# Optimization experiments

Hardware: AMD Instinct MI355X
Metric: run time of the kernel (lower is better)

## Reference

```python
import jax, jax.numpy as jnp
import numpy as np

N = 50000      # n_nodes
E = 600000     # n_edges (avg degree 12)
IN_DIM = 128
HID = 256
OUT = 2


def _glorot(k, fan_in, fan_out):
    s = jnp.sqrt(6.0 / (fan_in + fan_out))
    return jax.random.uniform(k, (fan_in, fan_out), jnp.float32, -s, s)


def setup_inputs() -> dict:
    key = jax.random.key(0)
    ks = jax.random.split(key, 6)
    x = jax.random.normal(ks[0], (N, IN_DIM), jnp.float32)
    edge_index = jax.random.randint(ks[1], (2, E), 0, N, jnp.int32)
    W1 = _glorot(ks[2], IN_DIM, HID)
    b1 = jnp.zeros((HID,), jnp.float32)
    W2 = _glorot(ks[3], HID, HID)
    b2 = jnp.zeros((HID,), jnp.float32)
    Wl = _glorot(ks[4], HID, OUT)
    bl = jnp.zeros((OUT,), jnp.float32)
    return {"x": x, "edge_index": edge_index, "W1": W1, "b1": b1,
            "W2": W2, "b2": b2, "Wl": Wl, "bl": bl}


def _gcn_conv(x, W, b, src, dst, dinv, n):
    # PyG GCNConv: transform, then propagate with symmetric norm + self-loops.
    h = x @ W                                   # [N, F_out]
    norm = (dinv[src] * dinv[dst])[:, None]     # [E, 1]
    agg = jax.ops.segment_sum(h[src] * norm, dst, num_segments=n)
    agg = agg + h * (dinv * dinv)[:, None]      # self-loop term: deg^-1 * h
    return agg + b


def reference(x, edge_index, W1, b1, W2, b2, Wl, bl):
    n = x.shape[0]
    src, dst = edge_index[0], edge_index[1]
    # degree (with self-loop) computed on destination nodes, as in PyG gcn_norm
    deg = jax.ops.segment_sum(jnp.ones((src.shape[0],), jnp.float32), dst,
                              num_segments=n) + 1.0
    dinv = jax.lax.rsqrt(deg)
    h = jax.nn.relu(_gcn_conv(x, W1, b1, src, dst, dinv, n))
    # dropout is identity in eval mode
    h = jax.nn.relu(_gcn_conv(h, W2, b2, src, dst, dinv, n))
    return h @ Wl + bl
```

## Files before the change

### kernel.cpp

```cpp
#include <hip/hip_runtime.h>
#include <hip/hip_bf16.h>
#include <hip/hip_fp16.h>

constexpr int IN_DIM = 128;
constexpr int HID    = 256;

typedef _Float16 f16x8 __attribute__((ext_vector_type(8)));
typedef float    f32x4 __attribute__((ext_vector_type(4)));


__global__ void zero_deg(int* __restrict__ deg, int n) {
    int i = blockIdx.x * blockDim.x + threadIdx.x;
    if (i < n) deg[i] = 0;
}

__device__ inline void conv_B_elem(const float* B, ushort* Bp, int id) {
    int k  = id >> 6;
    int n4 = (id & 63) * 4;
    float4 v = *(const float4*)(B + (size_t)k * 256 + n4);
    size_t base = (size_t)(k >> 5) * (256 * 32) + (k & 31);
    Bp[base + (size_t)(n4 + 0) * 32] = __half_as_ushort(__float2half(v.x));
    Bp[base + (size_t)(n4 + 1) * 32] = __half_as_ushort(__float2half(v.y));
    Bp[base + (size_t)(n4 + 2) * 32] = __half_as_ushort(__float2half(v.z));
    Bp[base + (size_t)(n4 + 3) * 32] = __half_as_ushort(__float2half(v.w));
}

__global__ void convert_count(const float* __restrict__ W1, ushort* __restrict__ B1p,
                              const float* __restrict__ W2, ushort* __restrict__ B2p,
                              const float* __restrict__ x, ushort* __restrict__ xh,
                              int total4, const int* __restrict__ dst,
                              int* __restrict__ rank, int* __restrict__ deg, int e) {
    int id = blockIdx.x * 256 + threadIdx.x;
    constexpr int C1 = IN_DIM * 64;
    constexpr int C2 = C1 + HID * 64;
    if (id < C1) {
        conv_B_elem(W1, B1p, id);
    } else if (id < C2) {
        conv_B_elem(W2, B2p, id - C1);
    } else if (id < C2 + total4) {
        int i = id - C2;
        float4 v = *(const float4*)(x + (size_t)i * 4);
        ushort4 o;
        o.x = __half_as_ushort(__float2half(v.x));
        o.y = __half_as_ushort(__float2half(v.y));
        o.z = __half_as_ushort(__float2half(v.z));
        o.w = __half_as_ushort(__float2half(v.w));
        *(ushort4*)(xh + (size_t)i * 4) = o;
    } else {
        int i = id - (C2 + total4);
        if (i < e) rank[i] = atomicAdd(&deg[dst[i]], 1);
    }
}

__global__ __launch_bounds__(256) void scan_partial(const int* __restrict__ deg,
                                                    int* __restrict__ escan,
                                                    int* __restrict__ blocksum,
                                                    float* __restrict__ dinv, int n) {
    __shared__ int lds[256];
    int t = threadIdx.x;
    int i = blockIdx.x * 256 + t;
    int v = (i < n) ? deg[i] : 0;
    if (i < n) dinv[i] = rsqrtf((float)v + 1.0f);
    lds[t] = v;
    __syncthreads();
    for (int off = 1; off < 256; off <<= 1) {
        int a = lds[t];
        int w = (t >= off) ? lds[t - off] : 0;
        __syncthreads();
        lds[t] = a + w;
        __syncthreads();
    }
    if (i < n) escan[i] = lds[t] - v;
    if (t == 255) blocksum[blockIdx.x] = lds[255];
}

__global__ __launch_bounds__(256) void scan_rest(const int* __restrict__ escan,
                                                 const int* __restrict__ blocksum,
                                                 int nb, int* __restrict__ rowptr, int n) {
    __shared__ int lds[256];
    int t = threadIdx.x;
    int v = (t < nb) ? blocksum[t] : 0;
    lds[t] = v;
    __syncthreads();
    for (int off = 1; off < 256; off <<= 1) {
        int a = lds[t];
        int w = (t >= off) ? lds[t - off] : 0;
        __syncthreads();
        lds[t] = a + w;
        __syncthreads();
    }
    int boff = (blockIdx.x > 0) ? lds[blockIdx.x - 1] : 0;
    int i = blockIdx.x * 256 + t;
    if (i < n) rowptr[i] = escan[i] + boff;
    if (blockIdx.x == 0 && t == 0) rowptr[n] = lds[nb - 1];
}

__global__ void scatter_edges(const int* __restrict__ src, const int* __restrict__ dst,
                              const int* __restrict__ rowptr,
                              const int* __restrict__ rank,
                              const float* __restrict__ dinv,
                              int2* __restrict__ esw, int e) {
    int i = blockIdx.x * blockDim.x + threadIdx.x;
    if (i < e) {
        int d = dst[i];
        int s = src[i];
        esw[rowptr[d] + rank[i]] = make_int2(s, __float_as_int(dinv[s] * dinv[d]));
    }
}

template <int K>
__global__ __launch_bounds__(256) void aggregate_p(const ushort* __restrict__ h,
                                                   const int* __restrict__ rowptr,
                                                   const int2* __restrict__ esw,
                                                   const float* __restrict__ dinv,
                                                   ushort* __restrict__ Pp,
                                                   int n, int Mp) {
    constexpr int VH = K / 64;
    int wid  = (blockIdx.x * 256 + threadIdx.x) >> 6;
    int lane = threadIdx.x & 63;
    if (wid >= n) return;
    float di = dinv[wid];
    float sw = di * di;
    float acc[VH];
    {
        const ushort* row = h + (size_t)wid * K + lane * VH;
        if constexpr (VH == 4) {
            uint2 u = *(const uint2*)row;
            float2 fa = __half22float2(*(__half2*)&u.x);
            float2 fb = __half22float2(*(__half2*)&u.y);
            acc[0] = fa.x * sw; acc[1] = fa.y * sw; acc[2] = fb.x * sw; acc[3] = fb.y * sw;
        } else {
            uint u = *(const uint*)row;
            float2 fa = __half22float2(*(__half2*)&u);
            acc[0] = fa.x * sw; acc[1] = fa.y * sw;
        }
    }
    int beg = rowptr[wid], fin = rowptr[wid + 1];
    for (int b = beg; b < fin; b += 64) {
        int cnt = fin - b;
        if (cnt > 64) cnt = 64;
        int2 pk = (lane < cnt) ? esw[b + lane] : make_int2(0, 0);
        int   sv = pk.x;
        float wv = __int_as_float(pk.y);
        int t = 0;
        for (; t + 8 <= cnt; t += 8) {
            float wr[8];
            if constexpr (VH == 4) {
                uint2 u[8];
#pragma unroll
                for (int k = 0; k < 8; k++) {
                    int s = __shfl(sv, t + k);
                    wr[k] = __shfl(wv, t + k);
                    u[k] = *(const uint2*)(h + (size_t)s * K + lane * VH);
                }
#pragma unroll
                for (int k = 0; k < 8; k++) {
                    float2 fa = __half22float2(*(__half2*)&u[k].x);
                    float2 fb = __half22float2(*(__half2*)&u[k].y);
                    acc[0] += fa.x * wr[k]; acc[1] += fa.y * wr[k];
                    acc[2] += fb.x * wr[k]; acc[3] += fb.y * wr[k];
                }
            } else {
                uint u[8];
#pragma unroll
                for (int k = 0; k < 8; k++) {
                    int s = __shfl(sv, t + k);
                    wr[k] = __shfl(wv, t + k);
                    u[k] = *(const uint*)(h + (size_t)s * K + lane * VH);
                }
#pragma unroll
                for (int k = 0; k < 8; k++) {
                    float2 fa = __half22float2(*(__half2*)&u[k]);
                    acc[0] += fa.x * wr[k]; acc[1] += fa.y * wr[k];
                }
            }
        }
        for (; t + 4 <= cnt; t += 4) {
            float wr[4];
            if constexpr (VH == 4) {
                uint2 u[4];
#pragma unroll
                for (int k = 0; k < 4; k++) {
                    int s = __shfl(sv, t + k);
                    wr[k] = __shfl(wv, t + k);
                    u[k] = *(const uint2*)(h + (size_t)s * K + lane * VH);
                }
#pragma unroll
                for (int k = 0; k < 4; k++) {
                    float2 fa = __half22float2(*(__half2*)&u[k].x);
                    float2 fb = __half22float2(*(__half2*)&u[k].y);
                    acc[0] += fa.x * wr[k]; acc[1] += fa.y * wr[k];
                    acc[2] += fb.x * wr[k]; acc[3] += fb.y * wr[k];
                }
            } else {
                uint u[4];
#pragma unroll
                for (int k = 0; k < 4; k++) {
                    int s = __shfl(sv, t + k);
                    wr[k] = __shfl(wv, t + k);
                    u[k] = *(const uint*)(h + (size_t)s * K + lane * VH);
                }
#pragma unroll
                for (int k = 0; k < 4; k++) {
                    float2 fa = __half22float2(*(__half2*)&u[k]);
                    acc[0] += fa.x * wr[k]; acc[1] += fa.y * wr[k];
                }
            }
        }
        for (; t < cnt; t++) {
            int   s = __shfl(sv, t);
            float w = __shfl(wv, t);
            const ushort* r = h + (size_t)s * K + lane * VH;
            if constexpr (VH == 4) {
                uint2 u = *(const uint2*)r;
                float2 fa = __half22float2(*(__half2*)&u.x);
                float2 fb = __half22float2(*(__half2*)&u.y);
                acc[0] += fa.x * w; acc[1] += fa.y * w;
                acc[2] += fb.x * w; acc[3] += fb.y * w;
            } else {
                uint u = *(const uint*)r;
                float2 fa = __half22float2(*(__half2*)&u);
                acc[0] += fa.x * w; acc[1] += fa.y * w;
            }
        }
    }
    int kglob = lane * VH;
    int chunk = kglob >> 5;
    int inner = kglob & 31;
    size_t base = (size_t)chunk * Mp * 32 + (size_t)wid * 32 + inner;
    if constexpr (VH == 4) {
        __half2 p0 = __floats2half2_rn(acc[0], acc[1]);
        __half2 p1 = __floats2half2_rn(acc[2], acc[3]);
        *(uint2*)&Pp[base] = make_uint2(*(uint*)&p0, *(uint*)&p1);
    } else {
        __half2 p0 = __floats2half2_rn(acc[0], acc[1]);
        *(uint*)&Pp[base] = *(uint*)&p0;
    }
}

template <int K, int MODE>
__global__ __launch_bounds__(256, 3) void gemm_f16(const ushort* __restrict__ Ap,
                                                   const ushort* __restrict__ Bp,
                                                   const float* __restrict__ bias,
                                                   ushort* __restrict__ C16,
                                                   const float* __restrict__ Wl,
                                                   const float* __restrict__ bl,
                                                   float* __restrict__ out,
                                                   int M, int Mp) {
    constexpr int NC = K / 32;
    __shared__ ushort Asm[NC * 1024];
    __shared__ ushort Bsm[2][8192];
    __shared__ float part[4][32][2];

    int tid  = threadIdx.x;
    int w    = tid >> 6;
    int lane = tid & 63;
    int l15  = lane & 15;
    int quad = lane >> 4;
    int row0 = blockIdx.x * 32;

    constexpr int TOTA = NC * 2;
    for (int j = w; j < TOTA; j += 4) {
        int c   = j >> 1;
        int sub = j & 1;
        const ushort* g = Ap + (size_t)c * Mp * 32 + (size_t)(row0 + sub * 16) * 32;
        ushort* l = Asm + c * 1024 + sub * 512;
        __builtin_amdgcn_global_load_lds(
            (const __attribute__((address_space(1))) uint*)(g + (size_t)lane * 8),
            (__attribute__((address_space(3))) uint*)l, 16, 0, 0);
    }
#pragma unroll
    for (int j = 0; j < 4; j++) {
        int seg = w * 4 + j;
        const ushort* g = Bp + (size_t)seg * 512;
        ushort* l = Bsm[0] + seg * 512;
        __builtin_amdgcn_global_load_lds(
            (const __attribute__((address_space(1))) uint*)(g + (size_t)lane * 8),
            (__attribute__((address_space(3))) uint*)l, 16, 0, 0);
    }

    f32x4 acc[2][4] = {};
#pragma unroll
    for (int c = 0; c < NC; c++) {
        __syncthreads();
        if (c + 1 < NC) {
            int nb_ = (c + 1) & 1;
#pragma unroll
            for (int j = 0; j < 4; j++) {
                int seg = w * 4 + j;
                const ushort* g = Bp + (size_t)(c + 1) * 8192 + (size_t)seg * 512;
                ushort* l = Bsm[nb_] + seg * 512;
                __builtin_amdgcn_global_load_lds(
                    (const __attribute__((address_space(1))) uint*)(g + (size_t)lane * 8),
                    (__attribute__((address_space(3))) uint*)l, 16, 0, 0);
            }
        }
        f16x8 fa[2], fb[4];
#pragma unroll
        for (int i = 0; i < 2; i++) {
            int off = c * 1024 + (i * 16 + l15) * 32 + quad * 8;
            fa[i] = *(const f16x8*)&Asm[off];
        }
#pragma unroll
        for (int j = 0; j < 4; j++) {
            int off = (w * 64 + j * 16 + l15) * 32 + quad * 8;
            fb[j] = *(const f16x8*)&Bsm[c & 1][off];
        }
#pragma unroll
        for (int i = 0; i < 2; i++)
#pragma unroll
            for (int j = 0; j < 4; j++)
                acc[i][j] = __builtin_amdgcn_mfma_f32_16x16x32_f16(fa[i], fb[j], acc[i][j], 0, 0, 0);
    }

    float bj[4];
#pragma unroll
    for (int j = 0; j < 4; j++) bj[j] = bias[w * 64 + j * 16 + l15];

    if constexpr (MODE == 1) {
#pragma unroll
        for (int i = 0; i < 2; i++)
#pragma unroll
            for (int reg = 0; reg < 4; reg++) {
                int r = row0 + i * 16 + quad * 4 + reg;
                if (r < M) {
                    ushort* cp = C16 + (size_t)r * 256 + w * 64 + l15;
#pragma unroll
                    for (int j = 0; j < 4; j++) {
                        float v = fmaxf(acc[i][j][reg] + bj[j], 0.f);
                        cp[j * 16] = __half_as_ushort(__float2half(v));
                    }
                }
            }
    } else {
        float wl0[4], wl1[4];
#pragma unroll
        for (int j = 0; j < 4; j++) {
            int cj = w * 64 + j * 16 + l15;
            float2 wv = *(const float2*)(Wl + cj * 2);
            wl0[j] = wv.x; wl1[j] = wv.y;
        }
#pragma unroll
        for (int i = 0; i < 2; i++)
#pragma unroll
            for (int reg = 0; reg < 4; reg++) {
                float s0 = 0.f, s1 = 0.f;
#pragma unroll
                for (int j = 0; j < 4; j++) {
                    float v = fmaxf(acc[i][j][reg] + bj[j], 0.f);
                    s0 += v * wl0[j];
                    s1 += v * wl1[j];
                }
#pragma unroll
                for (int off = 1; off < 16; off <<= 1) {
                    s0 += __shfl_xor(s0, off);
                    s1 += __shfl_xor(s1, off);
                }
                if (l15 == 0) {
                    int r = i * 16 + quad * 4 + reg;
                    part[w][r][0] = s0;
                    part[w][r][1] = s1;
                }
            }
        __syncthreads();
        if (tid < 64) {
            int r = tid >> 1, o = tid & 1;
            int grr = row0 + r;
            if (grr < M) {
                float s = part[0][r][o] + part[1][r][o] + part[2][r][o] + part[3][r][o] + bl[o];
                out[(size_t)grr * 2 + o] = s;
            }
        }
    }
}


extern "C" void kernel_launch(void* const* d_in, const int* in_sizes, int n_in,
                              void* d_out, int out_size, void* d_ws, size_t ws_size,
                              hipStream_t stream) {
    const float* x  = (const float*)d_in[0];
    const int*   ei = (const int*)d_in[1];
    const float* W1 = (const float*)d_in[2];
    const float* b1 = (const float*)d_in[3];
    const float* W2 = (const float*)d_in[4];
    const float* b2 = (const float*)d_in[5];
    const float* Wl = (const float*)d_in[6];
    const float* bl = (const float*)d_in[7];
    float* out = (float*)d_out;

    int n = in_sizes[0] / IN_DIM;
    int e = in_sizes[1] / 2;
    const int* src = ei;
    const int* dst = ei + e;

    int gblocks = (n + 31) / 32;
    int Mp = gblocks * 32;

    char* ws = (char*)d_ws;
    size_t off = 0;
    auto alloc = [&](size_t bytes) -> void* {
        void* p = ws + off;
        off += (bytes + 255) & ~(size_t)255;
        return p;
    };
    int*    deg    = (int*)alloc((size_t)n * 4);
    float*  dinv   = (float*)alloc((size_t)n * 4);
    int*    rowptr = (int*)alloc((size_t)(n + 1) * 4);
    int*    escan  = (int*)alloc((size_t)n * 4);
    int*    bsum   = (int*)alloc(256 * 4);
    int*    rank   = (int*)alloc((size_t)e * 4);
    int2*   esw    = (int2*)alloc((size_t)e * 8);
    ushort* xh     = (ushort*)alloc((size_t)n * IN_DIM * 2);
    ushort* h1     = (ushort*)alloc((size_t)n * HID * 2);
    ushort* A1p    = (ushort*)alloc((size_t)Mp * IN_DIM * 2);
    ushort* A2p    = (ushort*)alloc((size_t)Mp * HID * 2);
    ushort* B1p    = (ushort*)alloc((size_t)IN_DIM * 256 * 2);
    ushort* B2p    = (ushort*)alloc((size_t)HID * 256 * 2);

    int nb = (n + 255) / 256;
    int eb = (e + 255) / 256;

    zero_deg<<<nb, 256, 0, stream>>>(deg, n);

    int total4 = n * IN_DIM / 4;
    int citems = IN_DIM * 64 + HID * 64 + total4 + e;
    convert_count<<<(citems + 255) / 256, 256, 0, stream>>>(W1, B1p, W2, B2p, x, xh,
                                                            total4, dst, rank, deg, e);

    scan_partial<<<nb, 256, 0, stream>>>(deg, escan, bsum, dinv, n);
    scan_rest<<<nb, 256, 0, stream>>>(escan, bsum, nb, rowptr, n);
    scatter_edges<<<eb, 256, 0, stream>>>(src, dst, rowptr, rank, dinv, esw, e);

    aggregate_p<IN_DIM><<<(n + 3) / 4, 256, 0, stream>>>(xh, rowptr, esw, dinv,
                                                         A1p, n, Mp);
    gemm_f16<IN_DIM, 1><<<gblocks, 256, 0, stream>>>(A1p, B1p, b1, h1,
                                                     nullptr, nullptr, nullptr, n, Mp);

    aggregate_p<HID><<<(n + 3) / 4, 256, 0, stream>>>(h1, rowptr, esw, dinv,
                                                      A2p, n, Mp);
    gemm_f16<HID, 2><<<gblocks, 256, 0, stream>>>(A2p, B2p, b2, nullptr,
                                                  Wl, bl, out, n, Mp);
}
```

Before: 235.1 us.

## Use persistent GEMM with resident weights and factor edge norm into dinv

The GEMM kernels become persistent. Each block loads the whole weight matrix into LDS once, then loops over row tiles, double-buffering the A tiles in the first layer. This removes the repeated per-tile B streaming but lowers occupancy because of the larger LDS footprint. Edge weights are no longer precomputed per edge. The aggregation multiplies by dinv[src] gathered per edge and by dinv[dst] once at the end, which halves the edge array size at the cost of an extra random gather. zero_deg is replaced by a memset.

```diff
diff --git a/kernel.cpp b/kernel.cpp
--- a/kernel.cpp
+++ b/kernel.cpp
@@ -7,12 +7,6 @@
 
 typedef _Float16 f16x8 __attribute__((ext_vector_type(8)));
 typedef float    f32x4 __attribute__((ext_vector_type(4)));
-
-
-__global__ void zero_deg(int* __restrict__ deg, int n) {
-    int i = blockIdx.x * blockDim.x + threadIdx.x;
-    if (i < n) deg[i] = 0;
-}
 
 __device__ inline void conv_B_elem(const float* B, ushort* Bp, int id) {
     int k  = id >> 6;
@@ -95,23 +89,20 @@
     if (blockIdx.x == 0 && t == 0) rowptr[n] = lds[nb - 1];
 }
 
-__global__ void scatter_edges(const int* __restrict__ src, const int* __restrict__ dst,
-                              const int* __restrict__ rowptr,
-                              const int* __restrict__ rank,
-                              const float* __restrict__ dinv,
-                              int2* __restrict__ esw, int e) {
+__global__ void scatter_src(const int* __restrict__ src, const int* __restrict__ dst,
+                            const int* __restrict__ rowptr,
+                            const int* __restrict__ rank,
+                            int* __restrict__ esrc, int e) {
     int i = blockIdx.x * blockDim.x + threadIdx.x;
     if (i < e) {
-        int d = dst[i];
-        int s = src[i];
-        esw[rowptr[d] + rank[i]] = make_int2(s, __float_as_int(dinv[s] * dinv[d]));
+        esrc[rowptr[dst[i]] + rank[i]] = src[i];
     }
 }
 
 template <int K>
 __global__ __launch_bounds__(256) void aggregate_p(const ushort* __restrict__ h,
                                                    const int* __restrict__ rowptr,
-                                                   const int2* __restrict__ esw,
+                                                   const int* __restrict__ esrc,
                                                    const float* __restrict__ dinv,
                                                    ushort* __restrict__ Pp,
                                                    int n, int Mp) {
@@ -120,7 +111,6 @@
     int lane = threadIdx.x & 63;
     if (wid >= n) return;
     float di = dinv[wid];
-    float sw = di * di;
     float acc[VH];
     {
         const ushort* row = h + (size_t)wid * K + lane * VH;
@@ -128,20 +118,19 @@
             uint2 u = *(const uint2*)row;
             float2 fa = __half22float2(*(__half2*)&u.x);
             float2 fb = __half22float2(*(__half2*)&u.y);
-            acc[0] = fa.x * sw; acc[1] = fa.y * sw; acc[2] = fb.x * sw; acc[3] = fb.y * sw;
+            acc[0] = fa.x * di; acc[1] = fa.y * di; acc[2] = fb.x * di; acc[3] = fb.y * di;
         } else {
             uint u = *(const uint*)row;
             float2 fa = __half22float2(*(__half2*)&u);
-            acc[0] = fa.x * sw; acc[1] = fa.y * sw;
+            acc[0] = fa.x * di; acc[1] = fa.y * di;
         }
     }
     int beg = rowptr[wid], fin = rowptr[wid + 1];
     for (int b = beg; b < fin; b += 64) {
         int cnt = fin - b;
         if (cnt > 64) cnt = 64;
-        int2 pk = (lane < cnt) ? esw[b + lane] : make_int2(0, 0);
-        int   sv = pk.x;
-        float wv = __int_as_float(pk.y);
+        int   sv = (lane < cnt) ? esrc[b + lane] : 0;
+        float wv = (lane < cnt) ? dinv[sv] : 0.f;
         int t = 0;
         for (; t + 8 <= cnt; t += 8) {
             float wr[8];
@@ -224,6 +213,9 @@
             }
         }
     }
+#pragma unroll
+    for (int j = 0; j < VH; j++) acc[j] *= di;
+
     int kglob = lane * VH;
     int chunk = kglob >> 5;
     int inner = kglob & 31;
@@ -239,136 +231,133 @@
 }
 
 template <int K, int MODE>
-__global__ __launch_bounds__(256, 3) void gemm_f16(const ushort* __restrict__ Ap,
-                                                   const ushort* __restrict__ Bp,
-                                                   const float* __restrict__ bias,
-                                                   ushort* __restrict__ C16,
-                                                   const float* __restrict__ Wl,
-                                                   const float* __restrict__ bl,
-                                                   float* __restrict__ out,
-                                                   int M, int Mp) {
-    constexpr int NC = K / 32;
-    __shared__ ushort Asm[NC * 1024];
-    __shared__ ushort Bsm[2][8192];
-    __shared__ float part[4][32][2];
+__global__ __launch_bounds__(256, (MODE == 1) ? 2 : 1)
+void gemm_p(const ushort* __restrict__ Ap, const ushort* __restrict__ Bp,
+            const float* __restrict__ bias, ushort* __restrict__ C16,
+            const float* __restrict__ Wl, const float* __restrict__ bl,
+            float* __restrict__ out, int M, int Mp, int ntiles) {
+    constexpr int NC   = K / 32;
+    constexpr int NBUF = (MODE == 1) ? 2 : 1;
+    __shared__ ushort Bsm[NC * 8192];
+    __shared__ ushort Asm[NBUF][NC * 1024];
 
     int tid  = threadIdx.x;
     int w    = tid >> 6;
     int lane = tid & 63;
     int l15  = lane & 15;
     int quad = lane >> 4;
-    int row0 = blockIdx.x * 32;
-
-    constexpr int TOTA = NC * 2;
-    for (int j = w; j < TOTA; j += 4) {
-        int c   = j >> 1;
-        int sub = j & 1;
-        const ushort* g = Ap + (size_t)c * Mp * 32 + (size_t)(row0 + sub * 16) * 32;
-        ushort* l = Asm + c * 1024 + sub * 512;
+
+    for (int j = w; j < NC * 16; j += 4) {
+        const ushort* g = Bp + (size_t)j * 512;
         __builtin_amdgcn_global_load_lds(
             (const __attribute__((address_space(1))) uint*)(g + (size_t)lane * 8),
-            (__attribute__((address_space(3))) uint*)l, 16, 0, 0);
-    }
-#pragma unroll
-    for (int j = 0; j < 4; j++) {
-        int seg = w * 4 + j;
-        const ushort* g = Bp + (size_t)seg * 512;
-        ushort* l = Bsm[0] + seg * 512;
-        __builtin_amdgcn_global_load_lds(
-            (const __attribute__((address_space(1))) uint*)(g + (size_t)lane * 8),
-            (__attribute__((address_space(3))) uint*)l, 16, 0, 0);
-    }
-
-    f32x4 acc[2][4] = {};
-#pragma unroll
-    for (int c = 0; c < NC; c++) {
-        __syncthreads();
-        if (c + 1 < NC) {
-            int nb_ = (c + 1) & 1;
-#pragma unroll
-            for (int j = 0; j < 4; j++) {
-                int seg = w * 4 + j;
-                const ushort* g = Bp + (size_t)(c + 1) * 8192 + (size_t)seg * 512;
-                ushort* l = Bsm[nb_] + seg * 512;
-                __builtin_amdgcn_global_load_lds(
-                    (const __attribute__((address_space(1))) uint*)(g + (size_t)lane * 8),
-                    (__attribute__((address_space(3))) uint*)l, 16, 0, 0);
-            }
-        }
-        f16x8 fa[2], fb[4];
-#pragma unroll
-        for (int i = 0; i < 2; i++) {
-            int off = c * 1024 + (i * 16 + l15) * 32 + quad * 8;
-            fa[i] = *(const f16x8*)&Asm[off];
-        }
-#pragma unroll
-        for (int j = 0; j < 4; j++) {
-            int off = (w * 64 + j * 16 + l15) * 32 + quad * 8;
-            fb[j] = *(const f16x8*)&Bsm[c & 1][off];
-        }
-#pragma unroll
-        for (int i = 0; i < 2; i++)
-#pragma unroll
-            for (int j = 0; j < 4; j++)
-                acc[i][j] = __builtin_amdgcn_mfma_f32_16x16x32_f16(fa[i], fb[j], acc[i][j], 0, 0, 0);
-    }
+            (__attribute__((address_space(3))) uint*)(Bsm + j * 512), 16, 0, 0);
+    }
+
+    auto stageA = [&](ushort* dl, int t) {
+        int row0 = t * 32;
+        for (int j = w; j < NC * 2; j += 4) {
+            int c = j >> 1, sub = j & 1;
+            const ushort* g = Ap + (size_t)c * Mp * 32 + (size_t)(row0 + sub * 16) * 32;
+            __builtin_amdgcn_global_load_lds(
+                (const __attribute__((address_space(1))) uint*)(g + (size_t)lane * 8),
+                (__attribute__((address_space(3))) uint*)(dl + c * 1024 + sub * 512),
+                16, 0, 0);
+        }
+    };
 
     float bj[4];
 #pragma unroll
     for (int j = 0; j < 4; j++) bj[j] = bias[w * 64 + j * 16 + l15];
-
-    if constexpr (MODE == 1) {
-#pragma unroll
-        for (int i = 0; i < 2; i++)
-#pragma unroll
-            for (int reg = 0; reg < 4; reg++) {
-                int r = row0 + i * 16 + quad * 4 + reg;
-                if (r < M) {
-                    ushort* cp = C16 + (size_t)r * 256 + w * 64 + l15;
-#pragma unroll
-                    for (int j = 0; j < 4; j++) {
-                        float v = fmaxf(acc[i][j][reg] + bj[j], 0.f);
-                        cp[j * 16] = __half_as_ushort(__float2half(v));
-                    }
-                }
-            }
-    } else {
-        float wl0[4], wl1[4];
+    float wl0[4], wl1[4];
+    if constexpr (MODE == 2) {
 #pragma unroll
         for (int j = 0; j < 4; j++) {
             int cj = w * 64 + j * 16 + l15;
             float2 wv = *(const float2*)(Wl + cj * 2);
             wl0[j] = wv.x; wl1[j] = wv.y;
         }
-#pragma unroll
-        for (int i = 0; i < 2; i++)
-#pragma unroll
-            for (int reg = 0; reg < 4; reg++) {
-                float s0 = 0.f, s1 = 0.f;
-#pragma unroll
-                for (int j = 0; j < 4; j++) {
-                    float v = fmaxf(acc[i][j][reg] + bj[j], 0.f);
-                    s0 += v * wl0[j];
-                    s1 += v * wl1[j];
-                }
-#pragma unroll
-                for (int off = 1; off < 16; off <<= 1) {
-                    s0 += __shfl_xor(s0, off);
-                    s1 += __shfl_xor(s1, off);
-                }
-                if (l15 == 0) {
-                    int r = i * 16 + quad * 4 + reg;
-                    part[w][r][0] = s0;
-                    part[w][r][1] = s1;
-                }
-            }
+    }
+
+    int cur = 0;
+    if ((int)blockIdx.x < ntiles) stageA(Asm[0], blockIdx.x);
+
+    for (int t = blockIdx.x; t < ntiles; t += gridDim.x) {
         __syncthreads();
-        if (tid < 64) {
-            int r = tid >> 1, o = tid & 1;
-            int grr = row0 + r;
-            if (grr < M) {
-                float s = part[0][r][o] + part[1][r][o] + part[2][r][o] + part[3][r][o] + bl[o];
-                out[(size_t)grr * 2 + o] = s;
+        if constexpr (MODE == 1) {
+            if (t + (int)gridDim.x < ntiles) stageA(Asm[cur ^ 1], t + gridDim.x);
+        }
+        f32x4 acc[2][4] = {};
+#pragma unroll
+        for (int c = 0; c < NC; c++) {
+            f16x8 fa[2], fb[4];
+#pragma unroll
+            for (int i = 0; i < 2; i++) {
+                int off = c * 1024 + (i * 16 + l15) * 32 + quad * 8;
+                fa[i] = *(const f16x8*)&Asm[cur][off];
+            }
+#pragma unroll
+            for (int j = 0; j < 4; j++) {
+                int off = c * 8192 + (w * 64 + j * 16 + l15) * 32 + quad * 8;
+                fb[j] = *(const f16x8*)&Bsm[off];
+            }
+#pragma unroll
+            for (int i = 0; i < 2; i++)
+#pragma unroll
+                for (int j = 0; j < 4; j++)
+                    acc[i][j] = __builtin_amdgcn_mfma_f32_16x16x32_f16(fa[i], fb[j], acc[i][j], 0, 0, 0);
+        }
+
+        int row0 = t * 32;
+        if constexpr (MODE == 1) {
+#pragma unroll
+            for (int i = 0; i < 2; i++)
+#pragma unroll
+                for (int reg = 0; reg < 4; reg++) {
+                    int r = row0 + i * 16 + quad * 4 + reg;
+                    if (r < M) {
+                        ushort* cp = C16 + (size_t)r * 256 + w * 64 + l15;
+#pragma unroll
+                        for (int j = 0; j < 4; j++) {
+                            float v = fmaxf(acc[i][j][reg] + bj[j], 0.f);
+                            cp[j * 16] = __half_as_ushort(__float2half(v));
+                        }
+                    }
+                }
+            cur ^= 1;
+        } else {
+            __shared__ float part[4][32][2];
+#pragma unroll
+            for (int i = 0; i < 2; i++)
+#pragma unroll
+                for (int reg = 0; reg < 4; reg++) {
+                    float s0 = 0.f, s1 = 0.f;
+#pragma unroll
+                    for (int j = 0; j < 4; j++) {
+                        float v = fmaxf(acc[i][j][reg] + bj[j], 0.f);
+                        s0 += v * wl0[j];
+                        s1 += v * wl1[j];
+                    }
+#pragma unroll
+                    for (int off = 1; off < 16; off <<= 1) {
+                        s0 += __shfl_xor(s0, off);
+                        s1 += __shfl_xor(s1, off);
+                    }
+                    if (l15 == 0) {
+                        int r = i * 16 + quad * 4 + reg;
+                        part[w][r][0] = s0;
+                        part[w][r][1] = s1;
+                    }
+                }
+            __syncthreads();
+            if (t + (int)gridDim.x < ntiles) stageA(Asm[0], t + gridDim.x);
+            if (tid < 64) {
+                int r = tid >> 1, o = tid & 1;
+                int grr = row0 + r;
+                if (grr < M) {
+                    float s = part[0][r][o] + part[1][r][o] + part[2][r][o] + part[3][r][o] + bl[o];
+                    out[(size_t)grr * 2 + o] = s;
+                }
             }
         }
     }
@@ -409,7 +398,7 @@
     int*    escan  = (int*)alloc((size_t)n * 4);
     int*    bsum   = (int*)alloc(256 * 4);
     int*    rank   = (int*)alloc((size_t)e * 4);
-    int2*   esw    = (int2*)alloc((size_t)e * 8);
+    int*    esrc   = (int*)alloc((size_t)e * 4);
     ushort* xh     = (ushort*)alloc((size_t)n * IN_DIM * 2);
     ushort* h1     = (ushort*)alloc((size_t)n * HID * 2);
     ushort* A1p    = (ushort*)alloc((size_t)Mp * IN_DIM * 2);
@@ -420,7 +409,7 @@
     int nb = (n + 255) / 256;
     int eb = (e + 255) / 256;
 
-    zero_deg<<<nb, 256, 0, stream>>>(deg, n);
+    hipMemsetAsync(deg, 0, (size_t)n * 4, stream);
 
     int total4 = n * IN_DIM / 4;
     int citems = IN_DIM * 64 + HID * 64 + total4 + e;
@@ -429,15 +418,16 @@
 
     scan_partial<<<nb, 256, 0, stream>>>(deg, escan, bsum, dinv, n);
     scan_rest<<<nb, 256, 0, stream>>>(escan, bsum, nb, rowptr, n);
-    scatter_edges<<<eb, 256, 0, stream>>>(src, dst, rowptr, rank, dinv, esw, e);
-
-    aggregate_p<IN_DIM><<<(n + 3) / 4, 256, 0, stream>>>(xh, rowptr, esw, dinv,
+    scatter_src<<<eb, 256, 0, stream>>>(src, dst, rowptr, rank, esrc, e);
+
+    aggregate_p<IN_DIM><<<(n + 3) / 4, 256, 0, stream>>>(xh, rowptr, esrc, dinv,
                                                          A1p, n, Mp);
-    gemm_f16<IN_DIM, 1><<<gblocks, 256, 0, stream>>>(A1p, B1p, b1, h1,
-                                                     nullptr, nullptr, nullptr, n, Mp);
-
-    aggregate_p<HID><<<(n + 3) / 4, 256, 0, stream>>>(h1, rowptr, esw, dinv,
+    gemm_p<IN_DIM, 1><<<512, 256, 0, stream>>>(A1p, B1p, b1, h1,
+                                               nullptr, nullptr, nullptr,
+                                               n, Mp, gblocks);
+
+    aggregate_p<HID><<<(n + 3) / 4, 256, 0, stream>>>(h1, rowptr, esrc, dinv,
                                                       A2p, n, Mp);
-    gemm_f16<HID, 2><<<gblocks, 256, 0, stream>>>(A2p, B2p, b2, nullptr,
-                                                  Wl, bl, out, n, Mp);
-}
+    gemm_p<HID, 2><<<256, 256, 0, stream>>>(A2p, B2p, b2, nullptr,
+                                            Wl, bl, out, n, Mp, gblocks);
+}
```

Measured after the change: 236.8 us. No clear change (+0.8%).
